# Kernel optimization log

Measured on AMD Instinct MI355X. Metric: run time of the kernel, lower is better.

## Reference

```python
import jax, jax.numpy as jnp
import numpy as np

B, T, N, D = 4, 8, 128, 512
H = 8
DH = D // H            # 64
HALF = DH // 2         # 32
NUM_FEATS = 3
SH_HID = 16
NUM_COEFF = 4          # l=0 (1) + l=1 (3)
ROPE_BASE = 1000.0
EPS = 1e-6
Y0 = 0.28209479177387814   # 1/sqrt(4*pi)
Y1 = 0.4886025119029199    # sqrt(3/(4*pi))


def setup_inputs() -> dict:
    key = jax.random.key(0)
    ks = jax.random.split(key, 16)
    s = 0.02
    return {
        'x_0': jax.random.normal(ks[0], (B, T, N, D), jnp.float32),
        'v_0': jax.random.normal(ks[1], (B, T, N, D), jnp.float32),
        'concatenated_features': jax.random.normal(ks[2], (B, T, N, D), jnp.float32),
        'q_data': jax.random.normal(ks[3], (B, T, N, D), jnp.float32),
        'Wq': jax.random.normal(ks[4], (D, D), jnp.float32) * s,
        'bq': jnp.zeros((D,), jnp.float32),
        'Wkv': jax.random.normal(ks[5], (NUM_FEATS, D, 2 * D), jnp.float32) * s,
        'bkv': jnp.zeros((NUM_FEATS, 2 * D), jnp.float32),
        'Wo': jax.random.normal(ks[6], (D, D), jnp.float32) * s,
        'bo': jnp.zeros((D,), jnp.float32),
        'feature_weights': jax.random.normal(ks[7], (NUM_FEATS,), jnp.float32) * 0.1,
        'attention_denom': jnp.full((H,), float(DH), jnp.float32),
        'W1': jax.random.normal(ks[8], (NUM_COEFF, SH_HID), jnp.float32) * 0.3,
        'b1': jnp.zeros((SH_HID,), jnp.float32),
        'W2': jax.random.normal(ks[9], (SH_HID, SH_HID), jnp.float32) * 0.3,
        'b2': jnp.zeros((SH_HID,), jnp.float32),
        'W3': jax.random.normal(ks[10], (SH_HID, H), jnp.float32) * 0.3,
        'b3': jnp.zeros((H,), jnp.float32),
    }


def _rope(t):
    # t: [B, H, S, DH]; groups of N nodes share the same timestep, offsets = 0
    positions = jnp.repeat(jnp.arange(T, dtype=jnp.float32), N)  # [S]
    freqs = 1.0 / (ROPE_BASE ** (2.0 * jnp.arange(HALF, dtype=jnp.float32) / DH))
    angle = positions[:, None] * freqs[None, :]                  # [S, HALF]
    cos_t, sin_t = jnp.cos(angle), jnp.sin(angle)
    t1, t2 = t[..., 0::2], t[..., 1::2]
    r0 = t1 * cos_t - t2 * sin_t
    r1 = t1 * sin_t + t2 * cos_t
    return jnp.stack([r0, r1], axis=-1).reshape(t.shape)


def _sh_bias(coords3, W1, b1, W2, b2, W3, b3):
    # coords3: [B, S, 3] -> bias [B, H, S, S]
    rel = coords3[:, :, None, :] - coords3[:, None, :, :]        # [B,S,S,3]
    norm = jnp.linalg.norm(rel, axis=-1, keepdims=True)
    unit = rel / (norm + EPS)
    # e3nn l=1 component order is (y, z, x)
    sh = jnp.concatenate([
        jnp.full(unit.shape[:-1] + (1,), Y0, unit.dtype),
        Y1 * unit[..., jnp.array([1, 2, 0])],
    ], axis=-1)                                                  # [B,S,S,4]
    h = jax.nn.silu(sh @ W1 + b1)
    h = jax.nn.silu(h @ W2 + b2)
    bias = h @ W3 + b3                                           # [B,S,S,H]
    return jnp.transpose(bias, (0, 3, 1, 2))                     # [B,H,S,S]


def reference(x_0, v_0, concatenated_features, q_data, Wq, bq, Wkv, bkv, Wo, bo,
              feature_weights, attention_denom, W1, b1, W2, b2, W3, b3):
    S = T * N
    q = (q_data.reshape(B, S, D) @ Wq + bq).reshape(B, S, H, DH)
    q = _rope(jnp.transpose(q, (0, 2, 1, 3)))                    # [B,H,S,DH]

    bias = _sh_bias(x_0[..., :3].reshape(B, S, 3), W1, b1, W2, b2, W3, b3)
    gates = jax.nn.softmax(feature_weights)
    inv_denom = (1.0 / attention_denom)[None, :, None, None]

    out = jnp.zeros((B, H, S, DH), q.dtype)
    for i, feat in enumerate([x_0, v_0, concatenated_features]):
        kv = feat.reshape(B, S, D) @ Wkv[i] + bkv[i]             # [B,S,2D]
        k, v = kv[..., :D], kv[..., D:]
        k = _rope(jnp.transpose(k.reshape(B, S, H, DH), (0, 2, 1, 3)))
        v = jnp.transpose(v.reshape(B, S, H, DH), (0, 2, 1, 3))
        scores = jnp.einsum('bhqd,bhkd->bhqk', q, k) * inv_denom + bias
        attn = jax.nn.softmax(scores, axis=-1)                   # dropout=identity (eval)
        out = out + gates[i] * jnp.einsum('bhqk,bhkd->bhqd', attn, v)

    out = jnp.transpose(out, (0, 2, 1, 3)).reshape(B, S, D)
    return (out @ Wo + bo).reshape(B, T, N, D)
```

## Files before the change

### kernel.cpp

```cpp
#include <hip/hip_runtime.h>
#include <hip/hip_bf16.h>

typedef unsigned short u16;
typedef __attribute__((ext_vector_type(4))) float f32x4;
typedef __attribute__((ext_vector_type(8))) short v8s;
typedef __attribute__((ext_vector_type(4))) _Float16 h16x4;
typedef __attribute__((ext_vector_type(2))) unsigned int u32x2;

#define NB 4
#define NT 8
#define NN 128
#define ND 512
#define NH 8
#define NDH 64
#define NS 1024
#define LOG2E 1.4426950408889634f

static __device__ __forceinline__ u16 f2b(float f) {
  __hip_bfloat16 h = __float2bfloat16(f);
  return *reinterpret_cast<u16*>(&h);
}
static __device__ __forceinline__ float b2f(u16 u) {
  __hip_bfloat16 h;
  *reinterpret_cast<u16*>(&h) = u;
  return __bfloat162float(h);
}
static __device__ __forceinline__ unsigned int cvtpk(float lo, float hi) {
  unsigned int r;
  asm("v_cvt_pk_bf16_f32 %0, %1, %2" : "=v"(r) : "v"(lo), "v"(hi));
  return r;
}
static __device__ __forceinline__ float fexp2(float x) {
#if __has_builtin(__builtin_amdgcn_exp2f)
  return __builtin_amdgcn_exp2f(x);
#else
  return __expf(x * 0.6931471805599453f);
#endif
}
static __device__ __forceinline__ void gl16(const u16* g, u16* l) {
  __builtin_amdgcn_global_load_lds(
      (const __attribute__((address_space(1))) unsigned int*)g,
      (__attribute__((address_space(3))) unsigned int*)l, 16, 0, 0);
}
static __device__ __forceinline__ f32x4 mfma16(h16x4 a, h16x4 b, f32x4 c) {
#if __has_builtin(__builtin_amdgcn_mfma_f32_16x16x16f16)
  return __builtin_amdgcn_mfma_f32_16x16x16f16(a, b, c, 0, 0, 0);
#else
  f32x4 d;
  asm volatile("v_mfma_f32_16x16x16_f16 %0, %1, %2, %3\n\ts_nop 7\n\ts_nop 7"
               : "=v"(d)
               : "v"(a), "v"(b), "v"(c));
  return d;
#endif
}
static __device__ __forceinline__ float frcp(float x) { return __builtin_amdgcn_rcpf(x); }

__global__ void __launch_bounds__(256) cast4_kernel(const float* __restrict__ s0,
                                                    const float* __restrict__ s1,
                                                    const float* __restrict__ s2,
                                                    const float* __restrict__ s3,
                                                    u16* __restrict__ dst,
                                                    float* __restrict__ crd) {
  int blk = blockIdx.x;
  if (blk >= 4096) {
    for (int i = threadIdx.x; i < 4096; i += 256) {
      float4 v;
      v.x = s1[(size_t)i * ND + 0];
      v.y = s1[(size_t)i * ND + 1];
      v.z = s1[(size_t)i * ND + 2];
      v.w = 0.0f;
      reinterpret_cast<float4*>(crd)[i] = v;
    }
    return;
  }
  int seg = blk >> 10;
  const float* src = seg == 0 ? s0 : (seg == 1 ? s1 : (seg == 2 ? s2 : s3));
  int i = (blk & 1023) * 256 + threadIdx.x;
  const float4* s4 = reinterpret_cast<const float4*>(src) + (size_t)i * 2;
  float4 a = s4[0], b = s4[1];
  u16 r[8] = {f2b(a.x), f2b(a.y), f2b(a.z), f2b(a.w),
              f2b(b.x), f2b(b.y), f2b(b.z), f2b(b.w)};
  *reinterpret_cast<v8s*>(dst + (size_t)seg * 2097152 + (size_t)i * 8) =
      *reinterpret_cast<v8s*>(r);
}

__global__ void __launch_bounds__(256) transpose_all_kernel(const float* __restrict__ Wq,
                                                            const float* __restrict__ Wkv,
                                                            const float* __restrict__ Wo,
                                                            u16* __restrict__ Wqt,
                                                            u16* __restrict__ Wkvt,
                                                            u16* __restrict__ Wot) {
  __shared__ float t[32][33];
  int bid = blockIdx.x;
  const float* W;
  u16* Wt;
  int N, tt;
  if (bid < 256) {
    W = Wq; Wt = Wqt; N = 512; tt = bid;
  } else if (bid < 1792) {
    int f = (bid - 256) >> 9;
    tt = (bid - 256) & 511;
    W = Wkv + (size_t)f * 524288;
    Wt = Wkvt + (size_t)f * 524288;
    N = 1024;
  } else {
    W = Wo; Wt = Wot; N = 512; tt = bid - 1792;
  }
  int ntb = N >> 5;
  int nb = (tt % ntb) * 32, kb = (tt / ntb) * 32;
  int tx = threadIdx.x & 31, ty = threadIdx.x >> 5;
#pragma unroll
  for (int i = 0; i < 4; i++) {
    int r = ty + i * 8;
    t[r][tx] = W[(size_t)(kb + r) * N + nb + tx];
  }
  __syncthreads();
#pragma unroll
  for (int i = 0; i < 4; i++) {
    int r = ty + i * 8;
    Wt[(size_t)(nb + r) * 512 + kb + tx] = f2b(t[tx][r]);
  }
}

__global__ void __launch_bounds__(256) gemm_kernel(const u16* __restrict__ A,
                                                   const u16* __restrict__ Wt,
                                                   const float* __restrict__ bias,
                                                   const float* __restrict__ dnm,
                                                   u16* __restrict__ outK,
                                                   u16* __restrict__ outV,
                                                   float* __restrict__ outF,
                                                   int M, int N, int K, int mode, int f) {
  __shared__ __align__(16) u16 sbuf[2 * 8192];
  int bid = blockIdx.x;
  if (mode == 1) {
    f = bid >> 8;
    bid &= 255;
    A += (size_t)f * 2097152;
    Wt += (size_t)f * 524288;
    bias += f * 1024;
  }
  int nt = N >> 7;
  int by = bid / nt, bx = bid % nt;
  int tid = threadIdx.x;
  int lane = tid & 63, wave = tid >> 6;
  int g = lane >> 4, li = lane & 15;
  int wr = (wave & 1) * 64, wc = (wave >> 1) * 64;
  f32x4 acc[4][4] = {};
  const u16* srcs[4];
  int dsts[4];
#pragma unroll
  for (int j = 0; j < 4; j++) {
    int c = wave * 4 + j;
    if (c < 8)
      srcs[j] = A + (size_t)(by * 128 + c * 16 + li) * K + g * 8;
    else
      srcs[j] = Wt + (size_t)(bx * 128 + (c - 8) * 16 + li) * K + g * 8;
    dsts[j] = c * 512 + lane * 8;
  }
  int nsteps = K >> 5;
#pragma unroll
  for (int j = 0; j < 4; j++) gl16(srcs[j], sbuf + dsts[j]);
  for (int t = 0; t < nsteps; t++) {
    int p = t & 1;
    if (t < nsteps - 1) {
#pragma unroll
      for (int j = 0; j < 4; j++)
        gl16(srcs[j] + (t + 1) * 32, sbuf + (p ^ 1) * 8192 + dsts[j]);
      asm volatile("s_waitcnt vmcnt(4)" ::: "memory");
    } else {
      asm volatile("s_waitcnt vmcnt(0)" ::: "memory");
    }
    __builtin_amdgcn_s_barrier();
    __builtin_amdgcn_sched_barrier(0);
    const u16* bufb = sbuf + p * 8192;
    v8s a[4], b[4];
#pragma unroll
    for (int mi = 0; mi < 4; mi++)
      a[mi] = *reinterpret_cast<const v8s*>(bufb + ((wr >> 4) + mi) * 512 + lane * 8);
#pragma unroll
    for (int ni = 0; ni < 4; ni++)
      b[ni] = *reinterpret_cast<const v8s*>(bufb + 4096 + ((wc >> 4) + ni) * 512 + lane * 8);
    __builtin_amdgcn_s_setprio(1);
#pragma unroll
    for (int mi = 0; mi < 4; mi++)
#pragma unroll
      for (int ni = 0; ni < 4; ni++)
        acc[mi][ni] = __builtin_amdgcn_mfma_f32_16x16x32_bf16(a[mi], b[ni], acc[mi][ni], 0, 0, 0);
    __builtin_amdgcn_s_setprio(0);
    __builtin_amdgcn_s_barrier();
  }
#pragma unroll
  for (int mi = 0; mi < 4; mi++)
#pragma unroll
    for (int ni = 0; ni < 4; ni++) {
      int n = bx * 128 + wc + ni * 16 + li;
      float bn = bias[n];
      int mbase = by * 128 + wr + mi * 16 + 4 * g;
      bool isv = (mode == 1) && (n >= 512);
      if (mode == 2) {
#pragma unroll
        for (int r = 0; r < 4; r++)
          outF[(size_t)(mbase + r) * N + n] = acc[mi][ni][r] + bn;
      } else if (!isv) {
        int d = n & 63, h = (n & 511) >> 6;
        int j = d >> 1;
        float freq = __expf(-(float)j * 0.21586735246819178f);
        float sca = (mode == 0) ? frcp(dnm[h]) * LOG2E : 1.0f;
#pragma unroll
        for (int r = 0; r < 4; r++) {
          int mrow = mbase + r;
          int b = mrow >> 10, s = mrow & 1023;
          float val = acc[mi][ni][r] + bn;
          float partner = __shfl_xor(val, 1);
          float ang = (float)(s >> 7) * freq;
          float sn = __sinf(ang), cs = __cosf(ang);
          float res = (n & 1) ? (partner * sn + val * cs) : (val * cs - partner * sn);
          res *= sca;
          size_t idx;
          if (mode == 0)
            idx = ((size_t)(b * NH + h) * NS + s) * NDH + d;
          else
            idx = ((size_t)((f * NB + b) * NH + h) * NS + s) * NDH + d;
          outK[idx] = f2b(res);
        }
      } else {
        int vd = n - 512;
        int h = vd >> 6, d = vd & 63;
        int b = mbase >> 10, s0 = mbase & 1023;
        u16 pk[4];
#pragma unroll
        for (int r = 0; r < 4; r++) pk[r] = f2b(acc[mi][ni][r] + bn);
        u16* dst = outV + ((size_t)((f * NB + b) * NH + h) * NDH + d) * NS + s0;
        *reinterpret_cast<ushort4*>(dst) = *reinterpret_cast<ushort4*>(pk);
      }
    }
}

__global__ void __launch_bounds__(256) bias_kernel(const float* __restrict__ coords,
                                                   const float* __restrict__ W1,
                                                   const float* __restrict__ b1,
                                                   const float* __restrict__ W2,
                                                   const float* __restrict__ b2,
                                                   const float* __restrict__ W3,
                                                   const float* __restrict__ b3,
                                                   u16* __restrict__ biasF) {
  int wave = threadIdx.x >> 6, lane = threadIdx.x & 63;
  int g = lane >> 4, li = lane & 15;
  int id = blockIdx.x * 4 + wave;
  int kt = id & 31, qt = (id >> 5) & 63, b = id >> 11;
  const float Y0 = 0.28209479177387814f;
  const float Y1 = 0.4886025119029199f;

  h16x4 A1 = {}, A2, A3;
#pragma unroll
  for (int r = 0; r < 4; r++) {
    A1[r] = (g == 0) ? (_Float16)W1[r * 16 + li] : (_Float16)0.0f;
    A2[r] = (_Float16)W2[(4 * g + r) * 16 + li];
    A3[r] = (li < 8) ? (_Float16)(W3[(4 * g + r) * 8 + li] * LOG2E) : (_Float16)0.0f;
  }
  f32x4 b1g = reinterpret_cast<const f32x4*>(b1)[g];
  f32x4 b2g = reinterpret_cast<const f32x4*>(b2)[g];
  f32x4 b3g = {0.f, 0.f, 0.f, 0.f};
  if (g < 2) b3g = reinterpret_cast<const f32x4*>(b3)[g] * LOG2E;

  const float4* crd4 = reinterpret_cast<const float4*>(coords);
  float4 cq = crd4[b * NS + qt * 16 + li];
  f32x4 zero = {0.f, 0.f, 0.f, 0.f};

  for (int gkc = 0; gkc < 4; gkc++) {
    unsigned int resw[4][4];
    float prev[4];
#pragma unroll
    for (int j = 0; j < 8; j++) {
      int k = kt * 32 + (j >> 2) * 16 + gkc * 4 + (j & 3);
      float4 ck = crd4[b * NS + k];
      float rx = cq.x - ck.x;
      float ry = cq.y - ck.y;
      float rz = cq.z - ck.z;
      float d2 = rx * rx + ry * ry + rz * rz;
      float inv = __builtin_amdgcn_rsqf(fmaxf(d2, 1e-20f));
      h16x4 B1 = {};
      if (g == 0) {
        B1[0] = (_Float16)Y0;
        B1[1] = (_Float16)(Y1 * ry * inv);
        B1[2] = (_Float16)(Y1 * rz * inv);
        B1[3] = (_Float16)(Y1 * rx * inv);
      }
      f32x4 c1 = mfma16(A1, B1, zero);
      h16x4 B2;
#pragma unroll
      for (int r = 0; r < 4; r++) {
        float a = c1[r] + b1g[r];
        B2[r] = (_Float16)(a * frcp(1.0f + __expf(-a)));
      }
      f32x4 c2 = mfma16(A2, B2, zero);
      h16x4 B3;
#pragma unroll
      for (int r = 0; r < 4; r++) {
        float a = c2[r] + b2g[r];
        B3[r] = (_Float16)(a * frcp(1.0f + __expf(-a)));
      }
      f32x4 c3 = mfma16(A3, B3, zero);
#pragma unroll
      for (int r = 0; r < 4; r++) {
        float val = c3[r] + b3g[r];
        if (j & 1)
          resw[r][j >> 1] = cvtpk(prev[r], val);
        else
          prev[r] = val;
      }
    }
    if (g < 2) {
      size_t coff = ((size_t)(qt * 32 + kt) * 64 + gkc * 16 + li) * 8;
#pragma unroll
      for (int r = 0; r < 4; r++) {
        u16* dst = biasF + (size_t)(b * NH + 4 * g + r) * 1048576 + coff;
        *reinterpret_cast<uint4*>(dst) = *reinterpret_cast<uint4*>(resw[r]);
      }
    }
  }
}

#define ATTN_LDSB 12288
__global__ void __launch_bounds__(768, 6) attn_kernel(const u16* __restrict__ q,
                                                      const u16* __restrict__ kmat,
                                                      const u16* __restrict__ vt,
                                                      const u16* __restrict__ biasF,
                                                      const float* __restrict__ fw,
                                                      u16* __restrict__ attno) {
  __shared__ __align__(16) u16 sbuf[2 * ATTN_LDSB];
  int d = blockIdx.x;
  int x = d & 7, u = d >> 3;
  int bh = x * 4 + (u & 3);
  int qb = u >> 2;
  int h = bh & 7, b = bh >> 3;
  int wave = threadIdx.x >> 6, lane = threadIdx.x & 63;
  int g = lane >> 4, li = lane & 15;
  int ff = wave >> 2, qtl = wave & 3;
  int qt = qb * 4 + qtl;

  float f0 = fw[0], f1 = fw[1], f2v = fw[2];
  float mxg = fmaxf(fmaxf(f0, f1), f2v);
  float e0 = __expf(f0 - mxg), e1 = __expf(f1 - mxg), e2 = __expf(f2v - mxg);
  float es = e0 + e1 + e2;
  float gate = (ff == 0 ? e0 : (ff == 1 ? e1 : e2)) / es;

  const u16* qbase = q + ((size_t)bh * NS + qt * 16 + li) * NDH + g * 8;
  v8s qa0 = *reinterpret_cast<const v8s*>(qbase);
  v8s qa1 = *reinterpret_cast<const v8s*>(qbase + 32);
  const u16* bfrag = biasF + (size_t)bh * 1048576 + (size_t)qt * 16384;

  auto stage = [&](int kt, int p) {
    int k0 = kt * 32;
    u16* bufb = sbuf + p * ATTN_LDSB;
#pragma unroll
    for (int j = 0; j < 2; j++) {
      int c = wave * 2 + j;
      if (c < 12) {
        int cf = c >> 2, kks = (c >> 1) & 1, hf = c & 1;
        const u16* src = kmat + ((size_t)(cf * 32 + bh) * NS + k0 + kks * 16 + li) * NDH +
                         hf * 32 + g * 8;
        gl16(src, bufb + cf * 2048 + (c & 3) * 512 + lane * 8);
      } else {
        int cc = c - 12, cf = cc >> 2, ni = cc & 3;
        const u16* src = vt + ((size_t)(cf * 32 + bh) * NDH + ni * 16 + li) * NS + k0 + g * 8;
        gl16(src, bufb + 6144 + cf * 2048 + ni * 512 + lane * 8);
      }
    }
  };

  float m = 0.f;
  float lr = 0.f;
  f32x4 o[4] = {};
  f32x4 zero = {0.f, 0.f, 0.f, 0.f};
  int s0lane = ((g & 1) << 5) + li;
  int kksT = g >> 1;

  stage(0, 0);

  for (int t = 0; t < 32; t++) {
    int p = t & 1;
    v8s bb = *reinterpret_cast<const v8s*>(bfrag + ((size_t)t * 64 + lane) * 8);
    if (t < 31) {
      stage(t + 1, p ^ 1);
      asm volatile("s_waitcnt vmcnt(2)" ::: "memory");
    } else {
      asm volatile("s_waitcnt vmcnt(0)" ::: "memory");
    }
    __builtin_amdgcn_s_barrier();
    __builtin_amdgcn_sched_barrier(0);
    const u16* bufb = sbuf + p * ATTN_LDSB;
    v8s kf[2][2];
#pragma unroll
    for (int kks = 0; kks < 2; kks++)
#pragma unroll
      for (int hf = 0; hf < 2; hf++)
        kf[kks][hf] = *reinterpret_cast<const v8s*>(
            bufb + ff * 2048 + (kks * 2 + hf) * 512 + lane * 8);
    float pv[2][4];
    __builtin_amdgcn_s_setprio(1);
#pragma unroll
    for (int kks = 0; kks < 2; kks++) {
      f32x4 sc = __builtin_amdgcn_mfma_f32_16x16x32_bf16(kf[kks][0], qa0, zero, 0, 0, 0);
      sc = __builtin_amdgcn_mfma_f32_16x16x32_bf16(kf[kks][1], qa1, sc, 0, 0, 0);
#pragma unroll
      for (int r = 0; r < 4; r++)
        pv[kks][r] = sc[r] + b2f((u16)bb[kks * 4 + r]);
    }
    __builtin_amdgcn_s_setprio(0);
    float pmax = fmaxf(fmaxf(fmaxf(pv[0][0], pv[0][1]), pv[0][2]),
                       fmaxf(fmaxf(pv[0][3], pv[1][0]), pv[1][1]));
    pmax = fmaxf(fmaxf(pmax, pv[1][2]), pv[1][3]);
    if (!__all(pmax - m <= 11.0f)) {
      float rm = pmax;
      rm = fmaxf(rm, __shfl_xor(rm, 1));
      rm = fmaxf(rm, __shfl_xor(rm, 2));
      rm = fmaxf(rm, __shfl_xor(rm, 4));
      rm = fmaxf(rm, __shfl_xor(rm, 8));
      rm = fmaxf(rm, __shfl_xor(rm, 16));
      rm = fmaxf(rm, __shfl_xor(rm, 32));
      float sc2 = fexp2(m - rm);
      lr *= sc2;
#pragma unroll
      for (int ni = 0; ni < 4; ni++)
#pragma unroll
        for (int r = 0; r < 4; r++) o[ni][r] *= sc2;
      m = rm;
    }
    float p2[2][4];
#pragma unroll
    for (int kks = 0; kks < 2; kks++)
#pragma unroll
      for (int r = 0; r < 4; r++) {
        p2[kks][r] = fexp2(pv[kks][r] - m);
        lr += p2[kks][r];
      }
    unsigned int pA0 = cvtpk(p2[0][0], p2[0][1]);
    unsigned int pA1 = cvtpk(p2[0][2], p2[0][3]);
    unsigned int pB0 = cvtpk(p2[1][0], p2[1][1]);
    unsigned int pB1 = cvtpk(p2[1][2], p2[1][3]);
    int warr[4];
#if __has_builtin(__builtin_amdgcn_permlane32_swap) && \
    __has_builtin(__builtin_amdgcn_permlane16_swap)
    {
      u32x2 r0 = __builtin_amdgcn_permlane32_swap(pA0, pB0, false, false);
      u32x2 r1 = __builtin_amdgcn_permlane32_swap(pA1, pB1, false, false);
      u32x2 s0 = __builtin_amdgcn_permlane16_swap(r0[0], r0[1], false, false);
      u32x2 s1 = __builtin_amdgcn_permlane16_swap(r1[0], r1[1], false, false);
      warr[0] = s0[0];
      warr[1] = s1[0];
      warr[2] = s0[1];
      warr[3] = s1[1];
    }
#else
    {
      int a00 = __shfl((int)pA0, s0lane), a01 = __shfl((int)pA1, s0lane);
      int a10 = __shfl((int)pB0, s0lane), a11 = __shfl((int)pB1, s0lane);
      int c00 = __shfl((int)pA0, s0lane + 16), c01 = __shfl((int)pA1, s0lane + 16);
      int c10 = __shfl((int)pB0, s0lane + 16), c11 = __shfl((int)pB1, s0lane + 16);
      warr[0] = kksT ? a10 : a00;
      warr[1] = kksT ? a11 : a01;
      warr[2] = kksT ? c10 : c00;
      warr[3] = kksT ? c11 : c01;
    }
#endif
    v8s pa = *reinterpret_cast<v8s*>(warr);
    __builtin_amdgcn_s_setprio(1);
#pragma unroll
    for (int ni = 0; ni < 4; ni++) {
      v8s vb = *reinterpret_cast<const v8s*>(bufb + 6144 + ff * 2048 + ni * 512 + lane * 8);
      o[ni] = __builtin_amdgcn_mfma_f32_16x16x32_bf16(pa, vb, o[ni], 0, 0, 0);
    }
    __builtin_amdgcn_s_setprio(0);
    __builtin_amdgcn_s_barrier();
  }
  float l = lr;
  l += __shfl_xor(l, 16);
  l += __shfl_xor(l, 32);
  float scl = gate / l;
  float srow[4];
#pragma unroll
  for (int r = 0; r < 4; r++)
    srow[r] = __shfl(scl, (lane & 48) | (((lane >> 2) & 12) + r));
  float out[4][4];
#pragma unroll
  for (int ni = 0; ni < 4; ni++)
#pragma unroll
    for (int r = 0; r < 4; r++) out[ni][r] = o[ni][r] * srow[r];

  float* part = reinterpret_cast<float*>(sbuf);
  if (ff > 0) {
    int fq = (ff - 1) * 4 + qtl;
#pragma unroll
    for (int ni = 0; ni < 4; ni++)
#pragma unroll
      for (int r = 0; r < 4; r++)
        part[fq * 1088 + (4 * g + r) * 68 + ni * 16 + li] = out[ni][r];
  }
  __syncthreads();
  if (ff == 0) {
#pragma unroll
    for (int ni = 0; ni < 4; ni++)
#pragma unroll
      for (int r = 0; r < 4; r++) {
        float v = out[ni][r] + part[qtl * 1088 + (4 * g + r) * 68 + ni * 16 + li] +
                  part[(4 + qtl) * 1088 + (4 * g + r) * 68 + ni * 16 + li];
        attno[((size_t)(b * NS + qt * 16 + 4 * g + r)) * ND + h * NDH + ni * 16 + li] =
            f2b(v);
      }
  }
}

extern "C" void kernel_launch(void* const* d_in, const int* in_sizes, int n_in,
                              void* d_out, int out_size, void* d_ws, size_t ws_size,
                              hipStream_t stream) {
  const float* x0 = (const float*)d_in[0];
  const float* v0 = (const float*)d_in[1];
  const float* cf = (const float*)d_in[2];
  const float* qd = (const float*)d_in[3];
  const float* Wq = (const float*)d_in[4];
  const float* bq = (const float*)d_in[5];
  const float* Wkv = (const float*)d_in[6];
  const float* bkv = (const float*)d_in[7];
  const float* Wo = (const float*)d_in[8];
  const float* bo = (const float*)d_in[9];
  const float* fw = (const float*)d_in[10];
  const float* dnm = (const float*)d_in[11];
  const float* W1 = (const float*)d_in[12];
  const float* b1 = (const float*)d_in[13];
  const float* W2 = (const float*)d_in[14];
  const float* b2 = (const float*)d_in[15];
  const float* W3 = (const float*)d_in[16];
  const float* b3 = (const float*)d_in[17];

  char* ws = (char*)d_ws;
  size_t off = 0;
  auto alloc = [&](size_t bytes) -> void* {
    void* p = ws + off;
    off = (off + bytes + 255) & ~(size_t)255;
    return p;
  };
  const size_t E = 4096ull * 512;
  u16* Aq = (u16*)alloc(E * 2);
  u16* Af = (u16*)alloc(3 * E * 2);
  u16* Wqt = (u16*)alloc(262144ull * 2);
  u16* Wkvt = (u16*)alloc(3ull * 524288 * 2);
  u16* Wot = (u16*)alloc(262144ull * 2);
  float* crd = (float*)alloc(4096ull * 4 * 4);
  u16* qr = (u16*)alloc(E * 2);
  u16* kr = (u16*)alloc(3 * E * 2);
  u16* vtr = (u16*)alloc(3 * E * 2);
  u16* biasF = (u16*)alloc(33554432ull * 2);
  u16* attno = (u16*)alloc(E * 2);
  (void)ws_size; (void)in_sizes; (void)n_in; (void)out_size; (void)Af;

  cast4_kernel<<<4097, 256, 0, stream>>>(qd, x0, v0, cf, Aq, crd);
  transpose_all_kernel<<<2048, 256, 0, stream>>>(Wq, Wkv, Wo, Wqt, Wkvt, Wot);

  gemm_kernel<<<128, 256, 0, stream>>>(Aq, Wqt, bq, dnm, qr, nullptr, nullptr,
                                       4096, 512, 512, 0, 0);
  gemm_kernel<<<768, 256, 0, stream>>>(Af, Wkvt, bkv, nullptr, kr, vtr, nullptr,
                                       4096, 1024, 512, 1, 0);
  bias_kernel<<<2048, 256, 0, stream>>>(crd, W1, b1, W2, b2, W3, b3, biasF);
  attn_kernel<<<512, 768, 0, stream>>>(qr, kr, vtr, biasF, fw, attno);
  gemm_kernel<<<128, 256, 0, stream>>>(attno, Wot, bo, nullptr, nullptr, nullptr,
                                       (float*)d_out, 4096, 512, 512, 2, 0);
}
```

Measured before the change: 192.1 us.

## Merge Q GEMM, KV GEMM and bias MLP into one heterogeneous launch

Three separate launches (Q projection GEMM, KV projection GEMM and the spherical-harmonic bias MLP) are combined into a single kernel that dispatches by block index: the first 896 blocks do the GEMMs and the remaining 2048 compute the bias. This removes two launch gaps and lets the independent GEMM and bias work run concurrently on the GPU. The output projection becomes a dedicated kernel with constants fixed at compile time. The cost is that the bias blocks now carry the GEMM kernel's LDS allocation and register footprint, which may lower their occupancy.

```diff
diff --git a/kernel.cpp b/kernel.cpp
--- a/kernel.cpp
+++ b/kernel.cpp
@@ -122,23 +122,206 @@
   }
 }
 
-__global__ void __launch_bounds__(256) gemm_kernel(const u16* __restrict__ A,
-                                                   const u16* __restrict__ Wt,
-                                                   const float* __restrict__ bias,
-                                                   const float* __restrict__ dnm,
-                                                   u16* __restrict__ outK,
-                                                   u16* __restrict__ outV,
-                                                   float* __restrict__ outF,
-                                                   int M, int N, int K, int mode, int f) {
+__global__ void __launch_bounds__(256) mid_kernel(
+    const u16* __restrict__ Aq, const u16* __restrict__ Wqt,
+    const float* __restrict__ bq, const float* __restrict__ dnm,
+    u16* __restrict__ qr, const u16* __restrict__ Af,
+    const u16* __restrict__ Wkvt, const float* __restrict__ bkv,
+    u16* __restrict__ kr, u16* __restrict__ vtr,
+    const float* __restrict__ coords, const float* __restrict__ W1,
+    const float* __restrict__ b1, const float* __restrict__ W2,
+    const float* __restrict__ b2, const float* __restrict__ W3,
+    const float* __restrict__ b3, u16* __restrict__ biasF) {
   __shared__ __align__(16) u16 sbuf[2 * 8192];
+  int bid0 = blockIdx.x;
+  int tid = threadIdx.x;
+  int lane = tid & 63, wave = tid >> 6;
+  int g = lane >> 4, li = lane & 15;
+
+  if (bid0 < 896) {
+    int mode, f, bid, N;
+    const u16 *A, *Wt;
+    const float* bv;
+    if (bid0 < 128) {
+      mode = 0; f = 0; bid = bid0; N = 512; A = Aq; Wt = Wqt; bv = bq;
+    } else {
+      mode = 1;
+      int t = bid0 - 128;
+      f = t >> 8; bid = t & 255; N = 1024;
+      A = Af + (size_t)f * 2097152;
+      Wt = Wkvt + (size_t)f * 524288;
+      bv = bkv + f * 1024;
+    }
+    const int K = 512;
+    int nt = N >> 7;
+    int by = bid / nt, bx = bid % nt;
+    int wr = (wave & 1) * 64, wc = (wave >> 1) * 64;
+    f32x4 acc[4][4] = {};
+    const u16* srcs[4];
+    int dsts[4];
+#pragma unroll
+    for (int j = 0; j < 4; j++) {
+      int c = wave * 4 + j;
+      if (c < 8)
+        srcs[j] = A + (size_t)(by * 128 + c * 16 + li) * K + g * 8;
+      else
+        srcs[j] = Wt + (size_t)(bx * 128 + (c - 8) * 16 + li) * K + g * 8;
+      dsts[j] = c * 512 + lane * 8;
+    }
+#pragma unroll
+    for (int j = 0; j < 4; j++) gl16(srcs[j], sbuf + dsts[j]);
+    for (int t = 0; t < 16; t++) {
+      int p = t & 1;
+      if (t < 15) {
+#pragma unroll
+        for (int j = 0; j < 4; j++)
+          gl16(srcs[j] + (t + 1) * 32, sbuf + (p ^ 1) * 8192 + dsts[j]);
+        asm volatile("s_waitcnt vmcnt(4)" ::: "memory");
+      } else {
+        asm volatile("s_waitcnt vmcnt(0)" ::: "memory");
+      }
+      __builtin_amdgcn_s_barrier();
+      __builtin_amdgcn_sched_barrier(0);
+      const u16* bufb = sbuf + p * 8192;
+      v8s a[4], b[4];
+#pragma unroll
+      for (int mi = 0; mi < 4; mi++)
+        a[mi] = *reinterpret_cast<const v8s*>(bufb + ((wr >> 4) + mi) * 512 + lane * 8);
+#pragma unroll
+      for (int ni = 0; ni < 4; ni++)
+        b[ni] = *reinterpret_cast<const v8s*>(bufb + 4096 + ((wc >> 4) + ni) * 512 + lane * 8);
+      __builtin_amdgcn_s_setprio(1);
+#pragma unroll
+      for (int mi = 0; mi < 4; mi++)
+#pragma unroll
+        for (int ni = 0; ni < 4; ni++)
+          acc[mi][ni] =
+              __builtin_amdgcn_mfma_f32_16x16x32_bf16(a[mi], b[ni], acc[mi][ni], 0, 0, 0);
+      __builtin_amdgcn_s_setprio(0);
+      __builtin_amdgcn_s_barrier();
+    }
+#pragma unroll
+    for (int mi = 0; mi < 4; mi++)
+#pragma unroll
+      for (int ni = 0; ni < 4; ni++) {
+        int n = bx * 128 + wc + ni * 16 + li;
+        float bn = bv[n];
+        int mbase = by * 128 + wr + mi * 16 + 4 * g;
+        bool isv = (mode == 1) && (n >= 512);
+        if (!isv) {
+          int d = n & 63, h = (n & 511) >> 6;
+          int j = d >> 1;
+          float freq = __expf(-(float)j * 0.21586735246819178f);
+          float sca = (mode == 0) ? frcp(dnm[h]) * LOG2E : 1.0f;
+#pragma unroll
+          for (int r = 0; r < 4; r++) {
+            int mrow = mbase + r;
+            int b = mrow >> 10, s = mrow & 1023;
+            float val = acc[mi][ni][r] + bn;
+            float partner = __shfl_xor(val, 1);
+            float ang = (float)(s >> 7) * freq;
+            float sn = __sinf(ang), cs = __cosf(ang);
+            float res = (n & 1) ? (partner * sn + val * cs) : (val * cs - partner * sn);
+            res *= sca;
+            size_t idx;
+            if (mode == 0)
+              idx = ((size_t)(b * NH + h) * NS + s) * NDH + d;
+            else
+              idx = ((size_t)((f * NB + b) * NH + h) * NS + s) * NDH + d;
+            (mode == 0 ? qr : kr)[idx] = f2b(res);
+          }
+        } else {
+          int vd = n - 512;
+          int h = vd >> 6, d = vd & 63;
+          int b = mbase >> 10, s0 = mbase & 1023;
+          u16 pk[4];
+#pragma unroll
+          for (int r = 0; r < 4; r++) pk[r] = f2b(acc[mi][ni][r] + bn);
+          u16* dst = vtr + ((size_t)((f * NB + b) * NH + h) * NDH + d) * NS + s0;
+          *reinterpret_cast<ushort4*>(dst) = *reinterpret_cast<ushort4*>(pk);
+        }
+      }
+  } else {
+    int id = (bid0 - 896) * 4 + wave;
+    int kt = id & 31, qt = (id >> 5) & 63, b = id >> 11;
+    const float Y0 = 0.28209479177387814f;
+    const float Y1 = 0.4886025119029199f;
+    h16x4 A1 = {}, A2, A3;
+#pragma unroll
+    for (int r = 0; r < 4; r++) {
+      A1[r] = (g == 0) ? (_Float16)W1[r * 16 + li] : (_Float16)0.0f;
+      A2[r] = (_Float16)W2[(4 * g + r) * 16 + li];
+      A3[r] = (li < 8) ? (_Float16)(W3[(4 * g + r) * 8 + li] * LOG2E) : (_Float16)0.0f;
+    }
+    f32x4 b1g = reinterpret_cast<const f32x4*>(b1)[g];
+    f32x4 b2g = reinterpret_cast<const f32x4*>(b2)[g];
+    f32x4 b3g = {0.f, 0.f, 0.f, 0.f};
+    if (g < 2) b3g = reinterpret_cast<const f32x4*>(b3)[g] * LOG2E;
+    const float4* crd4 = reinterpret_cast<const float4*>(coords);
+    float4 cq = crd4[b * NS + qt * 16 + li];
+    f32x4 zero = {0.f, 0.f, 0.f, 0.f};
+    for (int gkc = 0; gkc < 4; gkc++) {
+      unsigned int resw[4][4];
+      float prev[4];
+#pragma unroll
+      for (int j = 0; j < 8; j++) {
+        int k = kt * 32 + (j >> 2) * 16 + gkc * 4 + (j & 3);
+        float4 ck = crd4[b * NS + k];
+        float rx = cq.x - ck.x;
+        float ry = cq.y - ck.y;
+        float rz = cq.z - ck.z;
+        float d2 = rx * rx + ry * ry + rz * rz;
+        float inv = __builtin_amdgcn_rsqf(fmaxf(d2, 1e-20f));
+        h16x4 B1 = {};
+        if (g == 0) {
+          B1[0] = (_Float16)Y0;
+          B1[1] = (_Float16)(Y1 * ry * inv);
+          B1[2] = (_Float16)(Y1 * rz * inv);
+          B1[3] = (_Float16)(Y1 * rx * inv);
+        }
+        f32x4 c1 = mfma16(A1, B1, zero);
+        h16x4 B2;
+#pragma unroll
+        for (int r = 0; r < 4; r++) {
+          float a = c1[r] + b1g[r];
+          B2[r] = (_Float16)(a * frcp(1.0f + __expf(-a)));
+        }
+        f32x4 c2 = mfma16(A2, B2, zero);
+        h16x4 B3;
+#pragma unroll
+        for (int r = 0; r < 4; r++) {
+          float a = c2[r] + b2g[r];
+          B3[r] = (_Float16)(a * frcp(1.0f + __expf(-a)));
+        }
+        f32x4 c3 = mfma16(A3, B3, zero);
+#pragma unroll
+        for (int r = 0; r < 4; r++) {
+          float val = c3[r] + b3g[r];
+          if (j & 1)
+            resw[r][j >> 1] = cvtpk(prev[r], val);
+          else
+            prev[r] = val;
+        }
+      }
+      if (g < 2) {
+        size_t coff = ((size_t)(qt * 32 + kt) * 64 + gkc * 16 + li) * 8;
+#pragma unroll
+        for (int r = 0; r < 4; r++) {
+          u16* dst = biasF + (size_t)(b * NH + 4 * g + r) * 1048576 + coff;
+          *reinterpret_cast<uint4*>(dst) = *reinterpret_cast<uint4*>(resw[r]);
+        }
+      }
+    }
+  }
+}
+
+__global__ void __launch_bounds__(256) gemm_out_kernel(const u16* __restrict__ A,
+                                                       const u16* __restrict__ Wt,
+                                                       const float* __restrict__ bias,
+                                                       float* __restrict__ outF) {
+  __shared__ __align__(16) u16 sbuf[2 * 8192];
+  const int N = 512, K = 512;
   int bid = blockIdx.x;
-  if (mode == 1) {
-    f = bid >> 8;
-    bid &= 255;
-    A += (size_t)f * 2097152;
-    Wt += (size_t)f * 524288;
-    bias += f * 1024;
-  }
   int nt = N >> 7;
   int by = bid / nt, bx = bid % nt;
   int tid = threadIdx.x;
@@ -157,12 +340,11 @@
       srcs[j] = Wt + (size_t)(bx * 128 + (c - 8) * 16 + li) * K + g * 8;
     dsts[j] = c * 512 + lane * 8;
   }
-  int nsteps = K >> 5;
 #pragma unroll
   for (int j = 0; j < 4; j++) gl16(srcs[j], sbuf + dsts[j]);
-  for (int t = 0; t < nsteps; t++) {
+  for (int t = 0; t < 16; t++) {
     int p = t & 1;
-    if (t < nsteps - 1) {
+    if (t < 15) {
 #pragma unroll
       for (int j = 0; j < 4; j++)
         gl16(srcs[j] + (t + 1) * 32, sbuf + (p ^ 1) * 8192 + dsts[j]);
@@ -196,129 +378,10 @@
       int n = bx * 128 + wc + ni * 16 + li;
       float bn = bias[n];
       int mbase = by * 128 + wr + mi * 16 + 4 * g;
-      bool isv = (mode == 1) && (n >= 512);
-      if (mode == 2) {
-#pragma unroll
-        for (int r = 0; r < 4; r++)
-          outF[(size_t)(mbase + r) * N + n] = acc[mi][ni][r] + bn;
-      } else if (!isv) {
-        int d = n & 63, h = (n & 511) >> 6;
-        int j = d >> 1;
-        float freq = __expf(-(float)j * 0.21586735246819178f);
-        float sca = (mode == 0) ? frcp(dnm[h]) * LOG2E : 1.0f;
-#pragma unroll
-        for (int r = 0; r < 4; r++) {
-          int mrow = mbase + r;
-          int b = mrow >> 10, s = mrow & 1023;
-          float val = acc[mi][ni][r] + bn;
-          float partner = __shfl_xor(val, 1);
-          float ang = (float)(s >> 7) * freq;
-          float sn = __sinf(ang), cs = __cosf(ang);
-          float res = (n & 1) ? (partner * sn + val * cs) : (val * cs - partner * sn);
-          res *= sca;
-          size_t idx;
-          if (mode == 0)
-            idx = ((size_t)(b * NH + h) * NS + s) * NDH + d;
-          else
-            idx = ((size_t)((f * NB + b) * NH + h) * NS + s) * NDH + d;
-          outK[idx] = f2b(res);
-        }
-      } else {
-        int vd = n - 512;
-        int h = vd >> 6, d = vd & 63;
-        int b = mbase >> 10, s0 = mbase & 1023;
-        u16 pk[4];
-#pragma unroll
-        for (int r = 0; r < 4; r++) pk[r] = f2b(acc[mi][ni][r] + bn);
-        u16* dst = outV + ((size_t)((f * NB + b) * NH + h) * NDH + d) * NS + s0;
-        *reinterpret_cast<ushort4*>(dst) = *reinterpret_cast<ushort4*>(pk);
-      }
-    }
-}
-
-__global__ void __launch_bounds__(256) bias_kernel(const float* __restrict__ coords,
-                                                   const float* __restrict__ W1,
-                                                   const float* __restrict__ b1,
-                                                   const float* __restrict__ W2,
-                                                   const float* __restrict__ b2,
-                                                   const float* __restrict__ W3,
-                                                   const float* __restrict__ b3,
-                                                   u16* __restrict__ biasF) {
-  int wave = threadIdx.x >> 6, lane = threadIdx.x & 63;
-  int g = lane >> 4, li = lane & 15;
-  int id = blockIdx.x * 4 + wave;
-  int kt = id & 31, qt = (id >> 5) & 63, b = id >> 11;
-  const float Y0 = 0.28209479177387814f;
-  const float Y1 = 0.4886025119029199f;
-
-  h16x4 A1 = {}, A2, A3;
-#pragma unroll
-  for (int r = 0; r < 4; r++) {
-    A1[r] = (g == 0) ? (_Float16)W1[r * 16 + li] : (_Float16)0.0f;
-    A2[r] = (_Float16)W2[(4 * g + r) * 16 + li];
-    A3[r] = (li < 8) ? (_Float16)(W3[(4 * g + r) * 8 + li] * LOG2E) : (_Float16)0.0f;
-  }
-  f32x4 b1g = reinterpret_cast<const f32x4*>(b1)[g];
-  f32x4 b2g = reinterpret_cast<const f32x4*>(b2)[g];
-  f32x4 b3g = {0.f, 0.f, 0.f, 0.f};
-  if (g < 2) b3g = reinterpret_cast<const f32x4*>(b3)[g] * LOG2E;
-
-  const float4* crd4 = reinterpret_cast<const float4*>(coords);
-  float4 cq = crd4[b * NS + qt * 16 + li];
-  f32x4 zero = {0.f, 0.f, 0.f, 0.f};
-
-  for (int gkc = 0; gkc < 4; gkc++) {
-    unsigned int resw[4][4];
-    float prev[4];
-#pragma unroll
-    for (int j = 0; j < 8; j++) {
-      int k = kt * 32 + (j >> 2) * 16 + gkc * 4 + (j & 3);
-      float4 ck = crd4[b * NS + k];
-      float rx = cq.x - ck.x;
-      float ry = cq.y - ck.y;
-      float rz = cq.z - ck.z;
-      float d2 = rx * rx + ry * ry + rz * rz;
-      float inv = __builtin_amdgcn_rsqf(fmaxf(d2, 1e-20f));
-      h16x4 B1 = {};
-      if (g == 0) {
-        B1[0] = (_Float16)Y0;
-        B1[1] = (_Float16)(Y1 * ry * inv);
-        B1[2] = (_Float16)(Y1 * rz * inv);
-        B1[3] = (_Float16)(Y1 * rx * inv);
-      }
-      f32x4 c1 = mfma16(A1, B1, zero);
-      h16x4 B2;
-#pragma unroll
-      for (int r = 0; r < 4; r++) {
-        float a = c1[r] + b1g[r];
-        B2[r] = (_Float16)(a * frcp(1.0f + __expf(-a)));
-      }
-      f32x4 c2 = mfma16(A2, B2, zero);
-      h16x4 B3;
-#pragma unroll
-      for (int r = 0; r < 4; r++) {
-        float a = c2[r] + b2g[r];
-        B3[r] = (_Float16)(a * frcp(1.0f + __expf(-a)));
-      }
-      f32x4 c3 = mfma16(A3, B3, zero);
-#pragma unroll
-      for (int r = 0; r < 4; r++) {
-        float val = c3[r] + b3g[r];
-        if (j & 1)
-          resw[r][j >> 1] = cvtpk(prev[r], val);
-        else
-          prev[r] = val;
-      }
-    }
-    if (g < 2) {
-      size_t coff = ((size_t)(qt * 32 + kt) * 64 + gkc * 16 + li) * 8;
-#pragma unroll
-      for (int r = 0; r < 4; r++) {
-        u16* dst = biasF + (size_t)(b * NH + 4 * g + r) * 1048576 + coff;
-        *reinterpret_cast<uint4*>(dst) = *reinterpret_cast<uint4*>(resw[r]);
-      }
-    }
-  }
+#pragma unroll
+      for (int r = 0; r < 4; r++)
+        outF[(size_t)(mbase + r) * N + n] = acc[mi][ni][r] + bn;
+    }
 }
 
 #define ATTN_LDSB 12288
@@ -556,13 +619,8 @@
 
   cast4_kernel<<<4097, 256, 0, stream>>>(qd, x0, v0, cf, Aq, crd);
   transpose_all_kernel<<<2048, 256, 0, stream>>>(Wq, Wkv, Wo, Wqt, Wkvt, Wot);
-
-  gemm_kernel<<<128, 256, 0, stream>>>(Aq, Wqt, bq, dnm, qr, nullptr, nullptr,
-                                       4096, 512, 512, 0, 0);
-  gemm_kernel<<<768, 256, 0, stream>>>(Af, Wkvt, bkv, nullptr, kr, vtr, nullptr,
-                                       4096, 1024, 512, 1, 0);
-  bias_kernel<<<2048, 256, 0, stream>>>(crd, W1, b1, W2, b2, W3, b3, biasF);
+  mid_kernel<<<2944, 256, 0, stream>>>(Aq, Wqt, bq, dnm, qr, Af, Wkvt, bkv, kr, vtr,
+                                       crd, W1, b1, W2, b2, W3, b3, biasF);
   attn_kernel<<<512, 768, 0, stream>>>(qr, kr, vtr, biasF, fw, attno);
-  gemm_kernel<<<128, 256, 0, stream>>>(attno, Wot, bo, nullptr, nullptr, nullptr,
-                                       (float*)d_out, 4096, 512, 512, 2, 0);
-}
+  gemm_out_kernel<<<128, 256, 0, stream>>>(attno, Wot, bo, (float*)d_out);
+}
```

After: 177.3 us. 1.08x faster.
